# Kernel tuning notes

Measured on AMD Instinct MI355X. Metric: run time of the kernel, lower is better.

## Reference

```python
import jax, jax.numpy as jnp
import numpy as np

N, M, E, HID, H = 50000, 4000, 320000, 128, 2
EPS = 1e-5  # torch BatchNorm1d eps


def _lrelu(x):
    return jnp.where(x >= 0, x, 0.2 * x)


def _bn(x, g, b):
    # BatchNorm1d in training mode: biased batch statistics over dim 0
    m = x.mean(0)
    v = ((x - m) ** 2).mean(0)
    return g * (x - m) * jax.lax.rsqrt(v + EPS) + b


def _seg_softmax(a, idx, n):
    # softmax of a[E,heads] normalized per node index idx (PyG softmax)
    mx = jax.ops.segment_max(a, idx, num_segments=n)
    e = jnp.exp(a - mx[idx])
    s = jax.ops.segment_sum(e, idx, num_segments=n)
    return e / s[idx]


def _hgconv(x, he_n, he_e, he_w, W, att, bias, heads):
    # PyG HypergraphConv(use_attention=True, concat=False)
    xl = (x @ W).reshape(N, heads, HID)                  # lin(x) -> [N,heads,C]
    # hyperedge_attr = incidence^T @ x  (matches to_dense_adj path in HGAT)
    ea = jax.ops.segment_sum(x[he_n], he_e, num_segments=M)  # [M,F]
    eal = (ea @ W).reshape(M, heads, HID)                # lin(hyperedge_attr)
    a = (jnp.concatenate([xl[he_n], eal[he_e]], axis=-1) * att[0]).sum(-1)  # [E,heads]
    a = _seg_softmax(_lrelu(a), he_n, N)
    # degree normalizations
    Dn = jax.ops.segment_sum(he_w[he_e], he_n, num_segments=N)
    Dinv = jnp.where(Dn > 0, 1.0 / Dn, 0.0)
    Bn = jax.ops.segment_sum(jnp.ones((E,), x.dtype), he_e, num_segments=M)
    Binv = jnp.where(Bn > 0, 1.0 / Bn, 0.0)
    # node -> hyperedge
    m1 = Binv[he_e][:, None, None] * xl[he_n] * a[..., None]
    eo = jax.ops.segment_sum(m1, he_e, num_segments=M)   # [M,heads,C]
    # hyperedge -> node
    m2 = Dinv[he_n][:, None, None] * eo[he_e] * a[..., None]
    out = jax.ops.segment_sum(m2, he_n, num_segments=N)  # [N,heads,C]
    return out.mean(1) + bias                            # concat=False -> head mean


def _forward(x, he_w, lin1_w, lin1_b, bn1_g, bn1_b, h1_w, h1_att, h1_b,
             bn2_g, bn2_b, h2_w, h2_att, h2_b, bn3_g, bn3_b,
             lin2_w, lin2_b, bn4_g, bn4_b, he_n, he_e):
    src = x
    x = _bn(_lrelu(x @ lin1_w + lin1_b), bn1_g, bn1_b)
    x2 = _hgconv(x, he_n, he_e, he_w, h1_w, h1_att, h1_b, H)
    x = _bn(x + x2, bn2_g, bn2_b)
    x2 = _hgconv(x, he_n, he_e, he_w, h2_w, h2_att, h2_b, 1)
    x = _bn(x + x2, bn3_g, bn3_b)
    x = _lrelu(x @ lin2_w + lin2_b)
    return _bn(src + x, bn4_g, bn4_b)


def setup_inputs() -> dict:
    key = jax.random.key(0)
    ks = jax.random.split(key, 10)
    s = 0.05
    he_n = jax.random.randint(ks[0], (E,), 0, N, dtype=jnp.int32)
    he_e = (jnp.arange(E, dtype=jnp.int32) % M)  # every hyperedge id used
    return {
        'x': jax.random.normal(ks[1], (N, 128), jnp.float32),
        'he_n': he_n, 'he_e': he_e,
        'he_w': jnp.ones((M,), jnp.float32),
        'lin1_w': jax.random.normal(ks[2], (128, HID), jnp.float32) * s,
        'lin1_b': jnp.zeros((HID,), jnp.float32),
        'bn1_g': jnp.ones((HID,), jnp.float32), 'bn1_b': jnp.zeros((HID,), jnp.float32),
        'h1_w': jax.random.normal(ks[3], (HID, H * HID), jnp.float32) * s,
        'h1_att': jax.random.normal(ks[4], (1, H, 2 * HID), jnp.float32) * s,
        'h1_b': jnp.zeros((HID,), jnp.float32),
        'bn2_g': jnp.ones((HID,), jnp.float32), 'bn2_b': jnp.zeros((HID,), jnp.float32),
        'h2_w': jax.random.normal(ks[5], (HID, HID), jnp.float32) * s,
        'h2_att': jax.random.normal(ks[6], (1, 1, 2 * HID), jnp.float32) * s,
        'h2_b': jnp.zeros((HID,), jnp.float32),
        'bn3_g': jnp.ones((HID,), jnp.float32), 'bn3_b': jnp.zeros((HID,), jnp.float32),
        'lin2_w': jax.random.normal(ks[7], (HID, 128), jnp.float32) * s,
        'lin2_b': jnp.zeros((128,), jnp.float32),
        'bn4_g': jnp.ones((128,), jnp.float32), 'bn4_b': jnp.zeros((128,), jnp.float32),
    }


def reference(x, he_n, he_e, he_w, lin1_w, lin1_b, bn1_g, bn1_b, h1_w, h1_att, h1_b,
              bn2_g, bn2_b, h2_w, h2_att, h2_b, bn3_g, bn3_b,
              lin2_w, lin2_b, bn4_g, bn4_b):
    return _forward(x, he_w, lin1_w, lin1_b, bn1_g, bn1_b, h1_w, h1_att, h1_b,
                    bn2_g, bn2_b, h2_w, h2_att, h2_b, bn3_g, bn3_b,
                    lin2_w, lin2_b, bn4_g, bn4_b, he_n, he_e)
```

## Files before the change

kernel.cpp:

```cpp
#include <hip/hip_runtime.h>
#include <math.h>

constexpr int Nn = 50000;
constexpr int Mm = 4000;
constexpr int Ee = 320000;
constexpr int KPB = Ee / Mm;
constexpr float BINV = 1.0f / (float)KPB;
constexpr float EPSf = 1e-5f;
constexpr int NBKT = 16;
constexpr int NBSCAN = 49;

__device__ __forceinline__ float lrelu_f(float x) { return x >= 0.f ? x : 0.2f * x; }

__device__ __forceinline__ float wave_sum(float v) {
#pragma unroll
    for (int o = 32; o >= 1; o >>= 1) v += __shfl_xor(v, o, 64);
    return v;
}

__device__ __forceinline__ void finalize_to_lds(const float* __restrict__ st,
                                                const float* __restrict__ g,
                                                const float* __restrict__ b,
                                                float* ABsh, int t) {
    if (t < 128) {
        double ds = 0, dq = 0;
#pragma unroll
        for (int i = 0; i < NBKT; i++) {
            ds += (double)st[i * 256 + t];
            dq += (double)st[i * 256 + 128 + t];
        }
        double mean = ds / (double)Nn;
        double var = dq / (double)Nn - mean * mean;
        float rstd = (float)(1.0 / sqrt(var + (double)EPSf));
        float A = g[t] * rstd;
        ABsh[t] = A;
        ABsh[128 + t] = b[t] - (float)mean * A;
    }
    __syncthreads();
}

__device__ void scan_body(const int* __restrict__ counts, int* __restrict__ offs,
                          int b, int t) {
    __shared__ int sdi[256];
    int pre = 0;
    for (int i = t; i < b * 1024; i += 256) pre += counts[i];
    sdi[t] = pre;
    __syncthreads();
    for (int st = 128; st >= 1; st >>= 1) {
        if (t < st) sdi[t] += sdi[t + st];
        __syncthreads();
    }
    int run0 = sdi[0];
    __syncthreads();
    int c4[4];
    int s = 0;
#pragma unroll
    for (int i = 0; i < 4; i++) {
        int n = b * 1024 + t * 4 + i;
        c4[i] = (n < Nn) ? counts[n] : 0;
        s += c4[i];
    }
    sdi[t] = s;
    __syncthreads();
    for (int off = 1; off < 256; off <<= 1) {
        int v = (t >= off) ? sdi[t - off] : 0;
        __syncthreads();
        sdi[t] += v;
        __syncthreads();
    }
    int run = sdi[t] - s + run0;
#pragma unroll
    for (int i = 0; i < 4; i++) {
        int n = b * 1024 + t * 4 + i;
        if (n < Nn) offs[n] = run;
        run += c4[i];
    }
    if (b == NBSCAN - 1 && t == 255) offs[Nn] = run0 + sdi[255];
}

template <int ROWS, bool LRELU, bool PROBN, bool RESID, bool STATS, bool PACKH2, bool SCANX>
__global__ __launch_bounds__(256) void gemmT(const float* __restrict__ A, size_t aystride,
                                             const float* __restrict__ B, int ldb,
                                             const float* __restrict__ bias, float scale,
                                             const float* __restrict__ stIn,
                                             const float* __restrict__ fing,
                                             const float* __restrict__ finb,
                                             const float* __restrict__ resid,
                                             float* __restrict__ stF,
                                             float* __restrict__ C, int ldc, int R,
                                             int gemmBlocksX,
                                             const int* __restrict__ counts,
                                             int* __restrict__ offs) {
    constexpr int RPT = ROWS / 16;
    const int t = threadIdx.x;
    if (SCANX && (int)blockIdx.x >= gemmBlocksX) {
        if (blockIdx.y == 0) scan_body(counts, offs, blockIdx.x - gemmBlocksX, t);
        return;
    }
    __shared__ float As[16][ROWS + 4];
    __shared__ float Bs[16][128];
    __shared__ float Sred[STATS ? 16 : 1][STATS ? 128 : 1];
    __shared__ float ABsh[PROBN ? 256 : 1];
    const int ty = t >> 4, tx = t & 15;
    const int row0 = blockIdx.x * ROWS;
    const int bcol = blockIdx.y * 128;
    A += (size_t)blockIdx.y * aystride;

    if (PROBN) finalize_to_lds(stIn, fing, finb, ABsh, t);

    float4 acc[RPT][2];
#pragma unroll
    for (int i = 0; i < RPT; i++)
#pragma unroll
        for (int q = 0; q < 2; q++) acc[i][q] = make_float4(0.f, 0.f, 0.f, 0.f);

    for (int k0 = 0; k0 < 128; k0 += 16) {
        if (ROWS == 64) {
            int r = t >> 2, kc = (t & 3) * 4;
            int rr = row0 + r;
            rr = rr < R ? rr : R - 1;
            float4 av = *(const float4*)(A + (size_t)rr * 128 + k0 + kc);
            if (PROBN) {
                float4 sA = *(const float4*)&ABsh[k0 + kc];
                float4 sB = *(const float4*)&ABsh[128 + k0 + kc];
                av.x = av.x * sA.x + sB.x; av.y = av.y * sA.y + sB.y;
                av.z = av.z * sA.z + sB.z; av.w = av.w * sA.w + sB.w;
            }
            As[kc + 0][r] = av.x; As[kc + 1][r] = av.y;
            As[kc + 2][r] = av.z; As[kc + 3][r] = av.w;
        } else {
            int r = t >> 3, kc = (t & 7) * 2;
            int rr = row0 + r;
            rr = rr < R ? rr : R - 1;
            float2 av = *(const float2*)(A + (size_t)rr * 128 + k0 + kc);
            if (PROBN) {
                av.x = av.x * ABsh[k0 + kc] + ABsh[128 + k0 + kc];
                av.y = av.y * ABsh[k0 + kc + 1] + ABsh[128 + k0 + kc + 1];
            }
            As[kc + 0][r] = av.x;
            As[kc + 1][r] = av.y;
        }
        {
            int kk = t >> 5, c4 = (t & 31) * 4;
            float4 bv0 = *(const float4*)(B + (size_t)(k0 + kk) * ldb + bcol + c4);
            float4 bv1 = *(const float4*)(B + (size_t)(k0 + kk + 8) * ldb + bcol + c4);
            *(float4*)&Bs[kk][c4] = bv0;
            *(float4*)&Bs[kk + 8][c4] = bv1;
        }
        __syncthreads();
#pragma unroll
        for (int kk = 0; kk < 16; kk++) {
            float ar[RPT];
            if (RPT == 4) {
                float4 a4 = *(const float4*)&As[kk][ty * 4];
                ar[0] = a4.x; ar[1] = a4.y; ar[2] = a4.z; ar[3] = a4.w;
            } else {
                float2 a2 = *(const float2*)&As[kk][ty * 2];
                ar[0] = a2.x; ar[RPT - 1] = a2.y;
            }
            float4 b0 = *(const float4*)&Bs[kk][4 * tx];
            float4 b1 = *(const float4*)&Bs[kk][64 + 4 * tx];
#pragma unroll
            for (int i = 0; i < RPT; i++) {
                acc[i][0].x = fmaf(ar[i], b0.x, acc[i][0].x);
                acc[i][0].y = fmaf(ar[i], b0.y, acc[i][0].y);
                acc[i][0].z = fmaf(ar[i], b0.z, acc[i][0].z);
                acc[i][0].w = fmaf(ar[i], b0.w, acc[i][0].w);
                acc[i][1].x = fmaf(ar[i], b1.x, acc[i][1].x);
                acc[i][1].y = fmaf(ar[i], b1.y, acc[i][1].y);
                acc[i][1].z = fmaf(ar[i], b1.z, acc[i][1].z);
                acc[i][1].w = fmaf(ar[i], b1.w, acc[i][1].w);
            }
        }
        __syncthreads();
    }

    float4 bv0 = make_float4(0.f, 0.f, 0.f, 0.f), bv1 = bv0;
    if (bias) {
        bv0 = *(const float4*)(bias + bcol + 4 * tx);
        bv1 = *(const float4*)(bias + bcol + 64 + 4 * tx);
    }
    float4 cs0 = make_float4(0.f, 0.f, 0.f, 0.f), cs1 = cs0, cq0 = cs0, cq1 = cs0;
#pragma unroll
    for (int i = 0; i < RPT; i++) {
        int row = row0 + ty * RPT + i;
        if (row >= R) continue;
        float4 v0, v1;
        v0.x = acc[i][0].x * scale + bv0.x; v0.y = acc[i][0].y * scale + bv0.y;
        v0.z = acc[i][0].z * scale + bv0.z; v0.w = acc[i][0].w * scale + bv0.w;
        v1.x = acc[i][1].x * scale + bv1.x; v1.y = acc[i][1].y * scale + bv1.y;
        v1.z = acc[i][1].z * scale + bv1.z; v1.w = acc[i][1].w * scale + bv1.w;
        if (LRELU) {
            v0.x = lrelu_f(v0.x); v0.y = lrelu_f(v0.y); v0.z = lrelu_f(v0.z); v0.w = lrelu_f(v0.w);
            v1.x = lrelu_f(v1.x); v1.y = lrelu_f(v1.y); v1.z = lrelu_f(v1.z); v1.w = lrelu_f(v1.w);
        }
        if (RESID) {
            float4 r0 = *(const float4*)(resid + (size_t)row * 128 + bcol + 4 * tx);
            float4 r1 = *(const float4*)(resid + (size_t)row * 128 + bcol + 64 + 4 * tx);
            v0.x += r0.x; v0.y += r0.y; v0.z += r0.z; v0.w += r0.w;
            v1.x += r1.x; v1.y += r1.y; v1.z += r1.z; v1.w += r1.w;
        }
        if (PACKH2) {
            int h = blockIdx.y;
            float* c0 = C + (size_t)row * ldc + 8 * tx + 2 * h;
            *(float2*)(c0) = make_float2(v0.x, v0.y);
            *(float2*)(c0 + 4) = make_float2(v0.z, v0.w);
            float* c1 = C + (size_t)row * ldc + 128 + 8 * tx + 2 * h;
            *(float2*)(c1) = make_float2(v1.x, v1.y);
            *(float2*)(c1 + 4) = make_float2(v1.z, v1.w);
        } else {
            *(float4*)(C + (size_t)row * ldc + bcol + 4 * tx) = v0;
            *(float4*)(C + (size_t)row * ldc + bcol + 64 + 4 * tx) = v1;
        }
        if (STATS) {
            cs0.x += v0.x; cs0.y += v0.y; cs0.z += v0.z; cs0.w += v0.w;
            cs1.x += v1.x; cs1.y += v1.y; cs1.z += v1.z; cs1.w += v1.w;
            cq0.x += v0.x * v0.x; cq0.y += v0.y * v0.y; cq0.z += v0.z * v0.z; cq0.w += v0.w * v0.w;
            cq1.x += v1.x * v1.x; cq1.y += v1.y * v1.y; cq1.z += v1.z * v1.z; cq1.w += v1.w * v1.w;
        }
    }
    if (STATS) {
        int bkt = blockIdx.x & (NBKT - 1);
#pragma unroll
        for (int pass = 0; pass < 2; pass++) {
            *(float4*)&Sred[ty][4 * tx] = pass ? cq0 : cs0;
            *(float4*)&Sred[ty][64 + 4 * tx] = pass ? cq1 : cs1;
            __syncthreads();
            if (t < 128) {
                float tot = 0.f;
#pragma unroll
                for (int r = 0; r < 16; r++) tot += Sred[r][t];
                atomicAdd(&stF[bkt * 256 + pass * 128 + t], tot);
            }
            __syncthreads();
        }
    }
}

__global__ void count_edges_watt(const int* __restrict__ he_n, int* __restrict__ counts,
                                 const float* __restrict__ h1_w, const float* __restrict__ h1_att,
                                 const float* __restrict__ h2_w, const float* __restrict__ h2_att,
                                 float* __restrict__ wnA, float* __restrict__ weA,
                                 int* __restrict__ he_nT) {
    int t = threadIdx.x;
    if (blockIdx.x == 1250) {
        for (int j = 0; j < 3; j++) {
            int id = t + 256 * j;
            if (id >= 768) break;
            int which = id / 384;
            int rem = id % 384;
            int h3 = rem >> 7, k = rem & 127;
            float s = 0.f;
            if (h3 < 2) {
                const float* wrow = h1_w + (size_t)k * 256 + h3 * 128;
                const float* arow = h1_att + h3 * 256 + which * 128;
                for (int c = 0; c < 128; c++) s += wrow[c] * arow[c];
            } else {
                const float* wrow = h2_w + (size_t)k * 128;
                const float* arow = h2_att + which * 128;
                for (int c = 0; c < 128; c++) s += wrow[c] * arow[c];
            }
            (which ? weA : wnA)[h3 * 128 + k] = s;
        }
        return;
    }
    int g = blockIdx.x * 256 + t;
    if (g < Ee) {
        int m = g / KPB;
        int k = g - m * KPB;
        int n = he_n[m + (size_t)k * Mm];
        he_nT[g] = n;
        atomicAdd(&counts[n], 1);
    }
}

template <int H, bool FILL>
__global__ __launch_bounds__(256) void bn_dots(const float* __restrict__ X,
                                               const float* __restrict__ stIn,
                                               const float* __restrict__ fing,
                                               const float* __restrict__ finb,
                                               float* __restrict__ ABout,
                                               const float* __restrict__ wn,
                                               const float* __restrict__ we,
                                               float* __restrict__ an,
                                               float* __restrict__ pe,
                                               const int* __restrict__ he_n,
                                               const int* __restrict__ offs,
                                               int* __restrict__ cursor,
                                               int* __restrict__ eid, int mainBlocks) {
    int t = threadIdx.x;
    if (FILL && (int)blockIdx.x >= mainBlocks) {
        int e = (blockIdx.x - mainBlocks) * 256 + t;
        if (e < Ee) {
            int n = he_n[e];
            int p = atomicAdd(&cursor[n], 1);
            eid[offs[n] + p] = e;
        }
        return;
    }
    __shared__ float ABsh[256];
    finalize_to_lds(stIn, fing, finb, ABsh, t);
    if (blockIdx.x == 0) ABout[t] = ABsh[t];
    int w = t >> 6, lane = t & 63;
    float a0 = ABsh[lane], a1 = ABsh[lane + 64];
    float b0 = ABsh[128 + lane], b1 = ABsh[192 + lane];
    float wn0[H], wn1[H], we0[H], we1[H];
#pragma unroll
    for (int h = 0; h < H; h++) {
        wn0[h] = wn[h * 128 + lane]; wn1[h] = wn[h * 128 + 64 + lane];
        we0[h] = we[h * 128 + lane]; we1[h] = we[h * 128 + 64 + lane];
    }
#pragma unroll
    for (int nn = 0; nn < 4; nn++) {
        int row = blockIdx.x * 16 + w * 4 + nn;
        const float* xr = X + (size_t)row * 128;
        float v0 = xr[lane] * a0 + b0;
        float v1 = xr[lane + 64] * a1 + b1;
        float pv[H], qv[H];
#pragma unroll
        for (int h = 0; h < H; h++) {
            pv[h] = wave_sum(v0 * wn0[h] + v1 * wn1[h]);
            qv[h] = wave_sum(v0 * we0[h] + v1 * we1[h]);
        }
        if (lane == 0) {
            if (H == 2) {
                *(float2*)&an[row * 2] = make_float2(pv[0], pv[1]);
                *(float2*)&pe[row * 2] = make_float2(qv[0], qv[1]);
            } else {
                an[row] = pv[0];
                pe[row] = qv[0];
            }
        }
    }
}

__global__ __launch_bounds__(256) void bn_out(const float* __restrict__ X,
                                              const float* __restrict__ stIn,
                                              const float* __restrict__ fing,
                                              const float* __restrict__ finb,
                                              float* __restrict__ Y) {
    __shared__ float ABsh[256];
    int t = threadIdx.x;
    finalize_to_lds(stIn, fing, finb, ABsh, t);
    int w = t >> 6, lane = t & 63;
    float a0 = ABsh[lane], a1 = ABsh[lane + 64];
    float b0 = ABsh[128 + lane], b1 = ABsh[192 + lane];
#pragma unroll
    for (int nn = 0; nn < 4; nn++) {
        int row = blockIdx.x * 16 + w * 4 + nn;
        const float* xr = X + (size_t)row * 128;
        float* yr = Y + (size_t)row * 128;
        yr[lane] = xr[lane] * a0 + b0;
        yr[lane + 64] = xr[lane + 64] * a1 + b1;
    }
}

template <int H>
__global__ __launch_bounds__(256) void ea_from_pe(const int* __restrict__ he_nT,
                                                  const float* __restrict__ pe,
                                                  float* __restrict__ ae) {
    int w = threadIdx.x >> 6, lane = threadIdx.x & 63;
    int m = blockIdx.x * 4 + w;
    if (m >= Mm) return;
    float s[H];
#pragma unroll
    for (int h = 0; h < H; h++) s[h] = 0.f;
    for (int k = lane; k < KPB; k += 64) {
        int idx = he_nT[m * KPB + k];
        if (H == 2) {
            float2 p2 = *(const float2*)(pe + (size_t)idx * 2);
            s[0] += p2.x;
            s[H - 1] += p2.y;
        } else {
            s[0] += pe[idx];
        }
    }
#pragma unroll
    for (int h = 0; h < H; h++) s[h] = wave_sum(s[h]);
    if (lane == 0)
#pragma unroll
        for (int h = 0; h < H; h++) ae[m * H + h] = s[h];
}

template <int H>
__global__ __launch_bounds__(256) void seg_softmax(const int* __restrict__ offs,
                                                   const int* __restrict__ eid,
                                                   const float* __restrict__ an,
                                                   const float* __restrict__ ae,
                                                   const float* __restrict__ he_w,
                                                   float* __restrict__ nsp) {
    int t = threadIdx.x;
    int wv = t >> 6, lane = t & 63;
    int q = lane >> 3, li = lane & 7;
    int n = blockIdx.x * 32 + wv * 8 + q;
    bool valid = n < Nn;
    int base = valid ? offs[n] : 0;
    int deg = valid ? offs[n + 1] - base : 0;
    float anv[H];
#pragma unroll
    for (int h = 0; h < H; h++) anv[h] = valid ? an[n * H + h] : 0.f;

    bool h0 = li < deg, h1 = li + 8 < deg;
    int m0 = 0, m1 = 0;
    float l0[H], l1[H];
    float mx[H];
#pragma unroll
    for (int h = 0; h < H; h++) { mx[h] = -INFINITY; l0[h] = 0.f; l1[h] = 0.f; }
    if (h0) {
        m0 = eid[base + li] % Mm;
#pragma unroll
        for (int h = 0; h < H; h++) {
            l0[h] = lrelu_f(anv[h] + ae[m0 * H + h]);
            mx[h] = fmaxf(mx[h], l0[h]);
        }
    }
    if (h1) {
        m1 = eid[base + li + 8] % Mm;
#pragma unroll
        for (int h = 0; h < H; h++) {
            l1[h] = lrelu_f(anv[h] + ae[m1 * H + h]);
            mx[h] = fmaxf(mx[h], l1[h]);
        }
    }
    for (int c = li + 16; c < deg; c += 8) {
        int m = eid[base + c] % Mm;
#pragma unroll
        for (int h = 0; h < H; h++) mx[h] = fmaxf(mx[h], lrelu_f(anv[h] + ae[m * H + h]));
    }
#pragma unroll
    for (int h = 0; h < H; h++) {
#pragma unroll
        for (int o = 1; o <= 4; o <<= 1) mx[h] = fmaxf(mx[h], __shfl_xor(mx[h], o, 64));
    }
    float sm[H];
#pragma unroll
    for (int h = 0; h < H; h++) sm[h] = 0.f;
    float dn = 0.f;
    if (h0) {
        dn += he_w[m0];
#pragma unroll
        for (int h = 0; h < H; h++) sm[h] += expf(l0[h] - mx[h]);
    }
    if (h1) {
        dn += he_w[m1];
#pragma unroll
        for (int h = 0; h < H; h++) sm[h] += expf(l1[h] - mx[h]);
    }
    for (int c = li + 16; c < deg; c += 8) {
        int m = eid[base + c] % Mm;
        dn += he_w[m];
#pragma unroll
        for (int h = 0; h < H; h++) sm[h] += expf(lrelu_f(anv[h] + ae[m * H + h]) - mx[h]);
    }
#pragma unroll
    for (int o = 1; o <= 4; o <<= 1) dn += __shfl_xor(dn, o, 64);
#pragma unroll
    for (int h = 0; h < H; h++) {
#pragma unroll
        for (int o = 1; o <= 4; o <<= 1) sm[h] += __shfl_xor(sm[h], o, 64);
    }
    if (valid && li == 0) {
        float Dv = dn > 0.f ? 1.0f / dn : 0.0f;
        if (H == 2) {
            *(float4*)(nsp + (size_t)n * 8) = make_float4(anv[0], anv[H - 1], mx[0], mx[H - 1]);
            *(float4*)(nsp + (size_t)n * 8 + 4) =
                make_float4(1.f / sm[0], 1.f / sm[H - 1], 0.5f * Dv, 0.f);
        } else {
            *(float4*)(nsp + (size_t)n * 4) = make_float4(anv[0], mx[0], 1.f / sm[0], Dv);
        }
    }
}

template <int H>
__global__ __launch_bounds__(256) void s_build(const float* __restrict__ X,
                                               const float* __restrict__ AB,
                                               const int* __restrict__ he_nT,
                                               const float* __restrict__ nsp,
                                               const float* __restrict__ ae,
                                               float* __restrict__ S) {
    __shared__ int idx[KPB];
    __shared__ float av[KPB][H];
    __shared__ float red[8][H][128];
    int m = blockIdx.x, t = threadIdx.x;
    int g = t >> 5, l = t & 31;
    if (t < KPB) {
        int nd = he_nT[m * KPB + t];
        idx[t] = nd;
        if (H == 2) {
            float4 pa = *(const float4*)(nsp + (size_t)nd * 8);
            float4 pb = *(const float4*)(nsp + (size_t)nd * 8 + 4);
            float2 a2 = *(const float2*)(ae + (size_t)m * 2);
            av[t][0] = expf(lrelu_f(pa.x + a2.x) - pa.z) * pb.x;
            av[t][H - 1] = expf(lrelu_f(pa.y + a2.y) - pa.w) * pb.y;
        } else {
            float4 pa = *(const float4*)(nsp + (size_t)nd * 4);
            float aem = ae[m];
            av[t][0] = expf(lrelu_f(pa.x + aem) - pa.y) * pa.z;
        }
    }
    __syncthreads();
    float4 A4 = ((const float4*)AB)[l];
    float4 B4 = ((const float4*)(AB + 128))[l];
    float4 acc[H];
#pragma unroll
    for (int h = 0; h < H; h++) acc[h] = make_float4(0.f, 0.f, 0.f, 0.f);
#pragma unroll
    for (int kk = 0; kk < KPB / 8; kk++) {
        int k = g + kk * 8;
        float4 v = ((const float4*)(X + (size_t)idx[k] * 128))[l];
        v.x = v.x * A4.x + B4.x;
        v.y = v.y * A4.y + B4.y;
        v.z = v.z * A4.z + B4.z;
        v.w = v.w * A4.w + B4.w;
#pragma unroll
        for (int h = 0; h < H; h++) {
            float a = av[k][h];
            acc[h].x = fmaf(a, v.x, acc[h].x);
            acc[h].y = fmaf(a, v.y, acc[h].y);
            acc[h].z = fmaf(a, v.z, acc[h].z);
            acc[h].w = fmaf(a, v.w, acc[h].w);
        }
    }
#pragma unroll
    for (int h = 0; h < H; h++) *(float4*)&red[g][h][l * 4] = acc[h];
    __syncthreads();
    if (t < 32 * H) {
        int h = t >> 5, l2 = t & 31;
        float4 s = make_float4(0.f, 0.f, 0.f, 0.f);
#pragma unroll
        for (int gg = 0; gg < 8; gg++) {
            float4 r = *(const float4*)&red[gg][h][l2 * 4];
            s.x += r.x; s.y += r.y; s.z += r.z; s.w += r.w;
        }
        ((float4*)(S + ((size_t)h * Mm + m) * 128))[l2] = s;
    }
}

template <int H>
__global__ __launch_bounds__(256) void node_agg(const int* __restrict__ offs,
                                                const int* __restrict__ eid,
                                                const float* __restrict__ nsp,
                                                const float* __restrict__ ae,
                                                const float* __restrict__ eo,
                                                const float* __restrict__ bias,
                                                const float* __restrict__ AB,
                                                float* __restrict__ stF,
                                                float* __restrict__ T) {
    __shared__ float smem[4][256];
    __shared__ float redS[4][128], redQ[4][128];
    int t = threadIdx.x;
    int w = t >> 6, lane = t & 63;
    int n0 = blockIdx.x * 16 + w * 4;
    int o = offs[n0 + (lane < 4 ? lane : 4)];
    int b0 = __shfl(o, 0, 64);
    int b1 = __shfl(o, 1, 64);
    int b2 = __shfl(o, 2, 64);
    int b3 = __shfl(o, 3, 64);
    int b4 = __shfl(o, 4, 64);
    int cnt = b4 - b0;
    int cnt64 = cnt < 64 ? cnt : 64;

    if (lane < cnt64) {
        int slot = b0 + lane;
        int j = (slot >= b1) + (slot >= b2) + (slot >= b3);
        int e = eid[slot];
        int m = e % Mm;
        if (H == 2) {
            float4 pa = *(const float4*)(nsp + (size_t)(n0 + j) * 8);
            float4 pb = *(const float4*)(nsp + (size_t)(n0 + j) * 8 + 4);
            float2 a2 = *(const float2*)(ae + (size_t)m * 2);
            float c0 = expf(lrelu_f(pa.x + a2.x) - pa.z) * pb.x * pb.z;
            float c1 = expf(lrelu_f(pa.y + a2.y) - pa.w) * pb.y * pb.z;
            *(float4*)&smem[w][4 * lane] = make_float4(__int_as_float(m), c0, c1, 0.f);
        } else {
            float4 pa = *(const float4*)(nsp + (size_t)(n0 + j) * 4);
            float c = expf(lrelu_f(pa.x + ae[m]) - pa.y) * pa.z * pa.w;
            *(float2*)&smem[w][2 * lane] = make_float2(__int_as_float(m), c);
        }
    }
    __syncthreads();

    int s1 = min(b1 - b0, cnt64), s2 = min(b2 - b0, cnt64), s3 = min(b3 - b0, cnt64);
    float2 acc0 = make_float2(0.f, 0.f), acc1 = acc0, acc2 = acc0, acc3 = acc0;

#define NA_BODY(ACC, CBEG, CEND)                                                \
    {                                                                           \
        int c = (CBEG);                                                         \
        for (; c + 1 < (CEND); c += 2) {                                        \
            if (H == 2) {                                                       \
                float4 sa = *(const float4*)&smem[w][4 * c];                    \
                float4 sb = *(const float4*)&smem[w][4 * (c + 1)];              \
                float4 ea = *(const float4*)(eo + (size_t)__float_as_int(sa.x) * 256 + 4 * lane); \
                float4 eb = *(const float4*)(eo + (size_t)__float_as_int(sb.x) * 256 + 4 * lane); \
                ACC.x += sa.y * ea.x + sa.z * ea.z + sb.y * eb.x + sb.z * eb.z; \
                ACC.y += sa.y * ea.y + sa.z * ea.w + sb.y * eb.y + sb.z * eb.w; \
            } else {                                                            \
                float2 sa = *(const float2*)&smem[w][2 * c];                    \
                float2 sb = *(const float2*)&smem[w][2 * (c + 1)];              \
                float2 ea = *(const float2*)(eo + (size_t)__float_as_int(sa.x) * 128 + 2 * lane); \
                float2 eb = *(const float2*)(eo + (size_t)__float_as_int(sb.x) * 128 + 2 * lane); \
                ACC.x += sa.y * ea.x + sb.y * eb.x;                             \
                ACC.y += sa.y * ea.y + sb.y * eb.y;                             \
            }                                                                   \
        }                                                                       \
        if (c < (CEND)) {                                                       \
            if (H == 2) {                                                       \
                float4 sa = *(const float4*)&smem[w][4 * c];                    \
                float4 ea = *(const float4*)(eo + (size_t)__float_as_int(sa.x) * 256 + 4 * lane); \
                ACC.x += sa.y * ea.x + sa.z * ea.z;                             \
                ACC.y += sa.y * ea.y + sa.z * ea.w;                             \
            } else {                                                            \
                float2 sa = *(const float2*)&smem[w][2 * c];                    \
                float2 ea = *(const float2*)(eo + (size_t)__float_as_int(sa.x) * 128 + 2 * lane); \
                ACC.x += sa.y * ea.x;                                           \
                ACC.y += sa.y * ea.y;                                           \
            }                                                                   \
        }                                                                       \
    }
    NA_BODY(acc0, 0, s1)
    NA_BODY(acc1, s1, s2)
    NA_BODY(acc2, s2, s3)
    NA_BODY(acc3, s3, cnt64)
#undef NA_BODY

    for (int ss = 64; ss < cnt; ss++) {
        int slot = b0 + ss;
        int j = (slot >= b1) + (slot >= b2) + (slot >= b3);
        int e = eid[slot];
        int m = e % Mm;
        float cx, cy;
        if (H == 2) {
            float4 pa = *(const float4*)(nsp + (size_t)(n0 + j) * 8);
            float4 pb = *(const float4*)(nsp + (size_t)(n0 + j) * 8 + 4);
            float2 a2 = *(const float2*)(ae + (size_t)m * 2);
            float c0 = expf(lrelu_f(pa.x + a2.x) - pa.z) * pb.x * pb.z;
            float c1 = expf(lrelu_f(pa.y + a2.y) - pa.w) * pb.y * pb.z;
            float4 ev = *(const float4*)(eo + (size_t)m * 256 + 4 * lane);
            cx = c0 * ev.x + c1 * ev.z;
            cy = c0 * ev.y + c1 * ev.w;
        } else {
            float4 pa = *(const float4*)(nsp + (size_t)(n0 + j) * 4);
            float c = expf(lrelu_f(pa.x + ae[m]) - pa.y) * pa.z * pa.w;
            float2 ev = *(const float2*)(eo + (size_t)m * 128 + 2 * lane);
            cx = c * ev.x;
            cy = c * ev.y;
        }
        if (j == 0) { acc0.x += cx; acc0.y += cy; }
        else if (j == 1) { acc1.x += cx; acc1.y += cy; }
        else if (j == 2) { acc2.x += cx; acc2.y += cy; }
        else { acc3.x += cx; acc3.y += cy; }
    }

    int col = 2 * lane;
    float2 A2 = *(const float2*)(AB + col);
    float2 B2 = *(const float2*)(AB + 128 + col);
    float2 bi = *(const float2*)(bias + col);
    float cs0 = 0.f, cs1 = 0.f, cq0 = 0.f, cq1 = 0.f;
    float2 accs[4] = {acc0, acc1, acc2, acc3};
#pragma unroll
    for (int j = 0; j < 4; j++) {
        int n = n0 + j;
        float2 xr = *(const float2*)(T + (size_t)n * 128 + col);
        float r0 = xr.x * A2.x + B2.x + bi.x + accs[j].x;
        float r1 = xr.y * A2.y + B2.y + bi.y + accs[j].y;
        *(float2*)(T + (size_t)n * 128 + col) = make_float2(r0, r1);
        cs0 += r0; cs1 += r1;
        cq0 += r0 * r0; cq1 += r1 * r1;
    }
    redS[w][col] = cs0; redS[w][col + 1] = cs1;
    redQ[w][col] = cq0; redQ[w][col + 1] = cq1;
    __syncthreads();
    if (t < 128) {
        float s = 0.f, qq = 0.f;
#pragma unroll
        for (int ww = 0; ww < 4; ww++) { s += redS[ww][t]; qq += redQ[ww][t]; }
        int bkt = blockIdx.x & (NBKT - 1);
        atomicAdd(&stF[bkt * 256 + t], s);
        atomicAdd(&stF[bkt * 256 + 128 + t], qq);
    }
}

extern "C" void kernel_launch(void* const* d_in, const int* in_sizes, int n_in,
                              void* d_out, int out_size, void* d_ws, size_t ws_size,
                              hipStream_t stream) {
    const float* x = (const float*)d_in[0];
    const int* he_n = (const int*)d_in[1];
    const float* he_w = (const float*)d_in[3];
    const float* lin1_w = (const float*)d_in[4];
    const float* lin1_b = (const float*)d_in[5];
    const float* bn1_g = (const float*)d_in[6];
    const float* bn1_b = (const float*)d_in[7];
    const float* h1_w = (const float*)d_in[8];
    const float* h1_att = (const float*)d_in[9];
    const float* h1_b = (const float*)d_in[10];
    const float* bn2_g = (const float*)d_in[11];
    const float* bn2_b = (const float*)d_in[12];
    const float* h2_w = (const float*)d_in[13];
    const float* h2_att = (const float*)d_in[14];
    const float* h2_b = (const float*)d_in[15];
    const float* bn3_g = (const float*)d_in[16];
    const float* bn3_b = (const float*)d_in[17];
    const float* lin2_w = (const float*)d_in[18];
    const float* lin2_b = (const float*)d_in[19];
    const float* bn4_g = (const float*)d_in[20];
    const float* bn4_b = (const float*)d_in[21];
    float* out = (float*)d_out;

    char* ws = (char*)d_ws;
    size_t off = 0;
    auto alloc = [&](size_t bytes) -> char* {
        char* p = ws + off;
        off = (off + bytes + 255) & ~(size_t)255;
        return p;
    };
    int* counts = (int*)alloc((size_t)Nn * 4);
    int* cursor = (int*)alloc((size_t)Nn * 4);
    float* stats = (float*)alloc((size_t)4 * NBKT * 256 * 4);
    size_t zbytes = off;
    int* offs = (int*)alloc((size_t)(Nn + 1) * 4);
    int* eid = (int*)alloc((size_t)Ee * 4);
    int* he_nT = (int*)alloc((size_t)Ee * 4);
    float* an = (float*)alloc((size_t)Nn * 2 * 4);
    float* pe = (float*)alloc((size_t)Nn * 2 * 4);
    float* ae = (float*)alloc((size_t)Mm * 2 * 4);
    float* nsp = (float*)alloc((size_t)Nn * 8 * 4);
    float* S = (float*)alloc((size_t)2 * Mm * 128 * 4);
    float* eo = (float*)alloc((size_t)2 * Mm * 128 * 4);
    float* wnA = (float*)alloc(384 * 4);
    float* weA = (float*)alloc(384 * 4);
    float* AB = (float*)alloc(2 * 256 * 4);
    float* buf = (float*)alloc((size_t)Nn * 128 * 4);

    float* st0 = stats;
    float* st1 = stats + NBKT * 256;
    float* st2 = stats + 2 * NBKT * 256;
    float* st3 = stats + 3 * NBKT * 256;
    float *AB1 = AB, *AB2 = AB + 256;

    hipMemsetAsync(d_ws, 0, zbytes, stream);

    constexpr int GB64 = (Nn + 63) / 64;
    count_edges_watt<<<1251, 256, 0, stream>>>(he_n, counts, h1_w, h1_att, h2_w, h2_att,
                                               wnA, weA, he_nT);

    gemmT<64, true, false, false, true, false, true><<<dim3(GB64 + NBSCAN, 1), 256, 0, stream>>>(
        x, 0, lin1_w, 128, lin1_b, 1.f, nullptr, nullptr, nullptr, nullptr, st0, buf, 128, Nn,
        GB64, counts, offs);
    bn_dots<2, true><<<3125 + 1250, 256, 0, stream>>>(buf, st0, bn1_g, bn1_b, AB1, wnA, weA,
                                                      an, pe, he_n, offs, cursor, eid, 3125);

    ea_from_pe<2><<<Mm / 4, 256, 0, stream>>>(he_nT, pe, ae);
    seg_softmax<2><<<(Nn + 31) / 32, 256, 0, stream>>>(offs, eid, an, ae, he_w, nsp);
    s_build<2><<<Mm, 256, 0, stream>>>(buf, AB1, he_nT, nsp, ae, S);
    gemmT<32, false, false, false, false, true, false><<<dim3(125, 2), 256, 0, stream>>>(
        S, (size_t)Mm * 128, h1_w, 256, nullptr, BINV, nullptr, nullptr, nullptr, nullptr,
        nullptr, eo, 256, Mm, 125, nullptr, nullptr);
    node_agg<2><<<3125, 256, 0, stream>>>(offs, eid, nsp, ae, eo, h1_b, AB1, st1, buf);

    bn_dots<1, false><<<3125, 256, 0, stream>>>(buf, st1, bn2_g, bn2_b, AB2, wnA + 256,
                                                weA + 256, an, pe, nullptr, nullptr, nullptr,
                                                nullptr, 3125);

    ea_from_pe<1><<<Mm / 4, 256, 0, stream>>>(he_nT, pe, ae);
    seg_softmax<1><<<(Nn + 31) / 32, 256, 0, stream>>>(offs, eid, an, ae, he_w, nsp);
    s_build<1><<<Mm, 256, 0, stream>>>(buf, AB2, he_nT, nsp, ae, S);
    gemmT<32, false, false, false, false, false, false><<<dim3(125, 1), 256, 0, stream>>>(
        S, 0, h2_w, 128, nullptr, BINV, nullptr, nullptr, nullptr, nullptr, nullptr,
        eo, 128, Mm, 125, nullptr, nullptr);
    node_agg<1><<<3125, 256, 0, stream>>>(offs, eid, nsp, ae, eo, h2_b, AB2, st2, buf);

    gemmT<64, true, true, true, true, false, false><<<dim3(GB64, 1), 256, 0, stream>>>(
        buf, 0, lin2_w, 128, lin2_b, 1.f, st2, bn3_g, bn3_b, x, st3, buf, 128, Nn,
        GB64, nullptr, nullptr);
    bn_out<<<3125, 256, 0, stream>>>(buf, st3, bn4_g, bn4_b, out);
}
```

Baseline: 395.8 us.

## Use split-bf16 MFMA for the two large node GEMMs

Replaces the FP32 SIMT tiled GEMM for lin1 and lin2 over 50000 rows with a matrix-core kernel. Activations are split on the fly into high and low bf16 parts and multiplied by pre-split, pre-swizzled weight fragments using three bf16 MFMAs, which approximates FP32 accuracy. The weight conversion runs in an extra block of the existing count kernel. Accuracy drops slightly versus true FP32, and C is written with scalar per-lane stores instead of float4 stores.

```diff
diff --git a/kernel.cpp b/kernel.cpp
--- a/kernel.cpp
+++ b/kernel.cpp
@@ -10,7 +10,15 @@
 constexpr int NBKT = 16;
 constexpr int NBSCAN = 49;
 
+typedef __attribute__((ext_vector_type(8))) short bfrag_t;
+typedef __attribute__((ext_vector_type(4))) float facc_t;
+
 __device__ __forceinline__ float lrelu_f(float x) { return x >= 0.f ? x : 0.2f * x; }
+
+__device__ __forceinline__ unsigned short f2bf(float f) {
+    unsigned int u = __float_as_uint(f);
+    return (unsigned short)((u + 0x7FFFu + ((u >> 16) & 1u)) >> 16);
+}
 
 __device__ __forceinline__ float wave_sum(float v) {
 #pragma unroll
@@ -78,36 +86,132 @@
     if (b == NBSCAN - 1 && t == 255) offs[Nn] = run0 + sdi[255];
 }
 
-template <int ROWS, bool LRELU, bool PROBN, bool RESID, bool STATS, bool PACKH2, bool SCANX>
-__global__ __launch_bounds__(256) void gemmT(const float* __restrict__ A, size_t aystride,
-                                             const float* __restrict__ B, int ldb,
-                                             const float* __restrict__ bias, float scale,
+template <bool LRELU, bool PROBN, bool RESID, bool STATS, bool SCANX>
+__global__ __launch_bounds__(256) void gemmM(const float* __restrict__ A,
+                                             const unsigned short* __restrict__ BH,
+                                             const unsigned short* __restrict__ BL,
+                                             const float* __restrict__ bias,
                                              const float* __restrict__ stIn,
                                              const float* __restrict__ fing,
                                              const float* __restrict__ finb,
                                              const float* __restrict__ resid,
                                              float* __restrict__ stF,
-                                             float* __restrict__ C, int ldc, int R,
+                                             float* __restrict__ C, int R,
                                              int gemmBlocksX,
                                              const int* __restrict__ counts,
                                              int* __restrict__ offs) {
+    const int t = threadIdx.x;
+    if (SCANX && (int)blockIdx.x >= gemmBlocksX) {
+        scan_body(counts, offs, blockIdx.x - gemmBlocksX, t);
+        return;
+    }
+    __shared__ float ABsh[PROBN ? 256 : 1];
+    __shared__ float SredS[STATS ? 4 : 1][STATS ? 128 : 1];
+    __shared__ float SredQ[STATS ? 4 : 1][STATS ? 128 : 1];
+    const int wv = t >> 6, l = t & 63, lm = l & 15, lg = l >> 4;
+    const int row0 = blockIdx.x * 64 + wv * 16;
+
+    if (PROBN) finalize_to_lds(stIn, fing, finb, ABsh, t);
+
+    int rA = row0 + lm;
+    rA = rA < R ? rA : R - 1;
+    const float* Ap = A + (size_t)rA * 128 + lg * 8;
+
+    facc_t acc[8];
+#pragma unroll
+    for (int ct = 0; ct < 8; ct++) acc[ct] = (facc_t){0.f, 0.f, 0.f, 0.f};
+
+#pragma unroll
+    for (int ks = 0; ks < 4; ks++) {
+        float4 a0 = *(const float4*)(Ap + ks * 32);
+        float4 a1 = *(const float4*)(Ap + ks * 32 + 4);
+        if (PROBN) {
+            const int cb = ks * 32 + lg * 8;
+            float4 cA0 = *(const float4*)&ABsh[cb];
+            float4 cA1 = *(const float4*)&ABsh[cb + 4];
+            float4 cB0 = *(const float4*)&ABsh[128 + cb];
+            float4 cB1 = *(const float4*)&ABsh[128 + cb + 4];
+            a0.x = a0.x * cA0.x + cB0.x; a0.y = a0.y * cA0.y + cB0.y;
+            a0.z = a0.z * cA0.z + cB0.z; a0.w = a0.w * cA0.w + cB0.w;
+            a1.x = a1.x * cA1.x + cB1.x; a1.y = a1.y * cA1.y + cB1.y;
+            a1.z = a1.z * cA1.z + cB1.z; a1.w = a1.w * cA1.w + cB1.w;
+        }
+        float av[8] = {a0.x, a0.y, a0.z, a0.w, a1.x, a1.y, a1.z, a1.w};
+        bfrag_t ah, al;
+#pragma unroll
+        for (int j = 0; j < 8; j++) {
+            unsigned short h = f2bf(av[j]);
+            float hf = __uint_as_float(((unsigned int)h) << 16);
+            ah[j] = (short)h;
+            al[j] = (short)f2bf(av[j] - hf);
+        }
+#pragma unroll
+        for (int ct = 0; ct < 8; ct++) {
+            const size_t fo = (((size_t)(ks * 8 + ct)) * 64 + l) * 8;
+            bfrag_t bh = *(const bfrag_t*)(BH + fo);
+            bfrag_t bl = *(const bfrag_t*)(BL + fo);
+            acc[ct] = __builtin_amdgcn_mfma_f32_16x16x32_bf16(ah, bh, acc[ct], 0, 0, 0);
+            acc[ct] = __builtin_amdgcn_mfma_f32_16x16x32_bf16(al, bh, acc[ct], 0, 0, 0);
+            acc[ct] = __builtin_amdgcn_mfma_f32_16x16x32_bf16(ah, bl, acc[ct], 0, 0, 0);
+        }
+    }
+
+    float cs[8], cq[8];
+#pragma unroll
+    for (int ct = 0; ct < 8; ct++) { cs[ct] = 0.f; cq[ct] = 0.f; }
+#pragma unroll
+    for (int ct = 0; ct < 8; ct++) {
+        const int col = ct * 16 + lm;
+        const float bv = bias ? bias[col] : 0.f;
+#pragma unroll
+        for (int r = 0; r < 4; r++) {
+            const int row = row0 + lg * 4 + r;
+            if (row >= R) continue;
+            float v = acc[ct][r] + bv;
+            if (LRELU) v = lrelu_f(v);
+            if (RESID) v += resid[(size_t)row * 128 + col];
+            C[(size_t)row * 128 + col] = v;
+            if (STATS) { cs[ct] += v; cq[ct] += v * v; }
+        }
+    }
+    if (STATS) {
+#pragma unroll
+        for (int ct = 0; ct < 8; ct++) {
+            cs[ct] += __shfl_xor(cs[ct], 16, 64);
+            cs[ct] += __shfl_xor(cs[ct], 32, 64);
+            cq[ct] += __shfl_xor(cq[ct], 16, 64);
+            cq[ct] += __shfl_xor(cq[ct], 32, 64);
+            if (lg == 0) {
+                SredS[wv][ct * 16 + lm] = cs[ct];
+                SredQ[wv][ct * 16 + lm] = cq[ct];
+            }
+        }
+        __syncthreads();
+        if (t < 128) {
+            float s = 0.f, q = 0.f;
+#pragma unroll
+            for (int ww = 0; ww < 4; ww++) { s += SredS[ww][t]; q += SredQ[ww][t]; }
+            int bkt = blockIdx.x & (NBKT - 1);
+            atomicAdd(&stF[bkt * 256 + t], s);
+            atomicAdd(&stF[bkt * 256 + 128 + t], q);
+        }
+    }
+}
+
+template <int ROWS, bool PACKH2>
+__global__ __launch_bounds__(256) void gemmT(const float* __restrict__ A, size_t aystride,
+                                             const float* __restrict__ B, int ldb,
+                                             float scale,
+                                             float* __restrict__ C, int ldc, int R) {
     constexpr int RPT = ROWS / 16;
     const int t = threadIdx.x;
-    if (SCANX && (int)blockIdx.x >= gemmBlocksX) {
-        if (blockIdx.y == 0) scan_body(counts, offs, blockIdx.x - gemmBlocksX, t);
-        return;
-    }
     __shared__ float As[16][ROWS + 4];
     __shared__ float Bs[16][128];
-    __shared__ float Sred[STATS ? 16 : 1][STATS ? 128 : 1];
-    __shared__ float ABsh[PROBN ? 256 : 1];
     const int ty = t >> 4, tx = t & 15;
     const int row0 = blockIdx.x * ROWS;
     const int bcol = blockIdx.y * 128;
     A += (size_t)blockIdx.y * aystride;
 
-    if (PROBN) finalize_to_lds(stIn, fing, finb, ABsh, t);
-
     float4 acc[RPT][2];
 #pragma unroll
     for (int i = 0; i < RPT; i++)
@@ -115,28 +219,11 @@
         for (int q = 0; q < 2; q++) acc[i][q] = make_float4(0.f, 0.f, 0.f, 0.f);
 
     for (int k0 = 0; k0 < 128; k0 += 16) {
-        if (ROWS == 64) {
-            int r = t >> 2, kc = (t & 3) * 4;
-            int rr = row0 + r;
-            rr = rr < R ? rr : R - 1;
-            float4 av = *(const float4*)(A + (size_t)rr * 128 + k0 + kc);
-            if (PROBN) {
-                float4 sA = *(const float4*)&ABsh[k0 + kc];
-                float4 sB = *(const float4*)&ABsh[128 + k0 + kc];
-                av.x = av.x * sA.x + sB.x; av.y = av.y * sA.y + sB.y;
-                av.z = av.z * sA.z + sB.z; av.w = av.w * sA.w + sB.w;
-            }
-            As[kc + 0][r] = av.x; As[kc + 1][r] = av.y;
-            As[kc + 2][r] = av.z; As[kc + 3][r] = av.w;
-        } else {
+        {
             int r = t >> 3, kc = (t & 7) * 2;
             int rr = row0 + r;
             rr = rr < R ? rr : R - 1;
             float2 av = *(const float2*)(A + (size_t)rr * 128 + k0 + kc);
-            if (PROBN) {
-                av.x = av.x * ABsh[k0 + kc] + ABsh[128 + k0 + kc];
-                av.y = av.y * ABsh[k0 + kc + 1] + ABsh[128 + k0 + kc + 1];
-            }
             As[kc + 0][r] = av.x;
             As[kc + 1][r] = av.y;
         }
@@ -151,10 +238,7 @@
 #pragma unroll
         for (int kk = 0; kk < 16; kk++) {
             float ar[RPT];
-            if (RPT == 4) {
-                float4 a4 = *(const float4*)&As[kk][ty * 4];
-                ar[0] = a4.x; ar[1] = a4.y; ar[2] = a4.z; ar[3] = a4.w;
-            } else {
+            {
                 float2 a2 = *(const float2*)&As[kk][ty * 2];
                 ar[0] = a2.x; ar[RPT - 1] = a2.y;
             }
@@ -175,31 +259,15 @@
         __syncthreads();
     }
 
-    float4 bv0 = make_float4(0.f, 0.f, 0.f, 0.f), bv1 = bv0;
-    if (bias) {
-        bv0 = *(const float4*)(bias + bcol + 4 * tx);
-        bv1 = *(const float4*)(bias + bcol + 64 + 4 * tx);
-    }
-    float4 cs0 = make_float4(0.f, 0.f, 0.f, 0.f), cs1 = cs0, cq0 = cs0, cq1 = cs0;
 #pragma unroll
     for (int i = 0; i < RPT; i++) {
         int row = row0 + ty * RPT + i;
         if (row >= R) continue;
         float4 v0, v1;
-        v0.x = acc[i][0].x * scale + bv0.x; v0.y = acc[i][0].y * scale + bv0.y;
-        v0.z = acc[i][0].z * scale + bv0.z; v0.w = acc[i][0].w * scale + bv0.w;
-        v1.x = acc[i][1].x * scale + bv1.x; v1.y = acc[i][1].y * scale + bv1.y;
-        v1.z = acc[i][1].z * scale + bv1.z; v1.w = acc[i][1].w * scale + bv1.w;
-        if (LRELU) {
-            v0.x = lrelu_f(v0.x); v0.y = lrelu_f(v0.y); v0.z = lrelu_f(v0.z); v0.w = lrelu_f(v0.w);
-            v1.x = lrelu_f(v1.x); v1.y = lrelu_f(v1.y); v1.z = lrelu_f(v1.z); v1.w = lrelu_f(v1.w);
-        }
-        if (RESID) {
-            float4 r0 = *(const float4*)(resid + (size_t)row * 128 + bcol + 4 * tx);
-            float4 r1 = *(const float4*)(resid + (size_t)row * 128 + bcol + 64 + 4 * tx);
-            v0.x += r0.x; v0.y += r0.y; v0.z += r0.z; v0.w += r0.w;
-            v1.x += r1.x; v1.y += r1.y; v1.z += r1.z; v1.w += r1.w;
-        }
+        v0.x = acc[i][0].x * scale; v0.y = acc[i][0].y * scale;
+        v0.z = acc[i][0].z * scale; v0.w = acc[i][0].w * scale;
+        v1.x = acc[i][1].x * scale; v1.y = acc[i][1].y * scale;
+        v1.z = acc[i][1].z * scale; v1.w = acc[i][1].w * scale;
         if (PACKH2) {
             int h = blockIdx.y;
             float* c0 = C + (size_t)row * ldc + 8 * tx + 2 * h;
@@ -212,28 +280,6 @@
             *(float4*)(C + (size_t)row * ldc + bcol + 4 * tx) = v0;
             *(float4*)(C + (size_t)row * ldc + bcol + 64 + 4 * tx) = v1;
         }
-        if (STATS) {
-            cs0.x += v0.x; cs0.y += v0.y; cs0.z += v0.z; cs0.w += v0.w;
-            cs1.x += v1.x; cs1.y += v1.y; cs1.z += v1.z; cs1.w += v1.w;
-            cq0.x += v0.x * v0.x; cq0.y += v0.y * v0.y; cq0.z += v0.z * v0.z; cq0.w += v0.w * v0.w;
-            cq1.x += v1.x * v1.x; cq1.y += v1.y * v1.y; cq1.z += v1.z * v1.z; cq1.w += v1.w * v1.w;
-        }
-    }
-    if (STATS) {
-        int bkt = blockIdx.x & (NBKT - 1);
-#pragma unroll
-        for (int pass = 0; pass < 2; pass++) {
-            *(float4*)&Sred[ty][4 * tx] = pass ? cq0 : cs0;
-            *(float4*)&Sred[ty][64 + 4 * tx] = pass ? cq1 : cs1;
-            __syncthreads();
-            if (t < 128) {
-                float tot = 0.f;
-#pragma unroll
-                for (int r = 0; r < 16; r++) tot += Sred[r][t];
-                atomicAdd(&stF[bkt * 256 + pass * 128 + t], tot);
-            }
-            __syncthreads();
-        }
     }
 }
 
@@ -241,7 +287,11 @@
                                  const float* __restrict__ h1_w, const float* __restrict__ h1_att,
                                  const float* __restrict__ h2_w, const float* __restrict__ h2_att,
                                  float* __restrict__ wnA, float* __restrict__ weA,
-                                 int* __restrict__ he_nT) {
+                                 int* __restrict__ he_nT,
+                                 const float* __restrict__ lin1_w,
+                                 const float* __restrict__ lin2_w,
+                                 unsigned short* __restrict__ bfH,
+                                 unsigned short* __restrict__ bfL) {
     int t = threadIdx.x;
     if (blockIdx.x == 1250) {
         for (int j = 0; j < 3; j++) {
@@ -261,6 +311,21 @@
                 for (int c = 0; c < 128; c++) s += wrow[c] * arow[c];
             }
             (which ? weA : wnA)[h3 * 128 + k] = s;
+        }
+        return;
+    }
+    if (blockIdx.x == 1251) {
+        for (int q = t; q < 32768; q += 256) {
+            int mat = q >> 14;
+            int e = q & 16383;
+            int j = e & 7, lane = (e >> 3) & 63, ct = (e >> 9) & 7, ks = e >> 12;
+            int k = ks * 32 + (lane >> 4) * 8 + j;
+            int n = ct * 16 + (lane & 15);
+            float f = (mat ? lin2_w : lin1_w)[(size_t)k * 128 + n];
+            unsigned short h = f2bf(f);
+            float hf = __uint_as_float(((unsigned int)h) << 16);
+            bfH[mat * 16384 + e] = h;
+            bfL[mat * 16384 + e] = f2bf(f - hf);
         }
         return;
     }
@@ -729,6 +794,8 @@
     float* wnA = (float*)alloc(384 * 4);
     float* weA = (float*)alloc(384 * 4);
     float* AB = (float*)alloc(2 * 256 * 4);
+    unsigned short* bfH = (unsigned short*)alloc((size_t)2 * 16384 * 2);
+    unsigned short* bfL = (unsigned short*)alloc((size_t)2 * 16384 * 2);
     float* buf = (float*)alloc((size_t)Nn * 128 * 4);
 
     float* st0 = stats;
@@ -739,22 +806,21 @@
 
     hipMemsetAsync(d_ws, 0, zbytes, stream);
 
-    constexpr int GB64 = (Nn + 63) / 64;
-    count_edges_watt<<<1251, 256, 0, stream>>>(he_n, counts, h1_w, h1_att, h2_w, h2_att,
-                                               wnA, weA, he_nT);
-
-    gemmT<64, true, false, false, true, false, true><<<dim3(GB64 + NBSCAN, 1), 256, 0, stream>>>(
-        x, 0, lin1_w, 128, lin1_b, 1.f, nullptr, nullptr, nullptr, nullptr, st0, buf, 128, Nn,
-        GB64, counts, offs);
+    constexpr int GB64M = (Nn + 63) / 64;
+    count_edges_watt<<<1252, 256, 0, stream>>>(he_n, counts, h1_w, h1_att, h2_w, h2_att,
+                                               wnA, weA, he_nT, lin1_w, lin2_w, bfH, bfL);
+
+    gemmM<true, false, false, true, true><<<GB64M + NBSCAN, 256, 0, stream>>>(
+        x, bfH, bfL, lin1_b, nullptr, nullptr, nullptr, nullptr, st0, buf, Nn,
+        GB64M, counts, offs);
     bn_dots<2, true><<<3125 + 1250, 256, 0, stream>>>(buf, st0, bn1_g, bn1_b, AB1, wnA, weA,
                                                       an, pe, he_n, offs, cursor, eid, 3125);
 
     ea_from_pe<2><<<Mm / 4, 256, 0, stream>>>(he_nT, pe, ae);
     seg_softmax<2><<<(Nn + 31) / 32, 256, 0, stream>>>(offs, eid, an, ae, he_w, nsp);
     s_build<2><<<Mm, 256, 0, stream>>>(buf, AB1, he_nT, nsp, ae, S);
-    gemmT<32, false, false, false, false, true, false><<<dim3(125, 2), 256, 0, stream>>>(
-        S, (size_t)Mm * 128, h1_w, 256, nullptr, BINV, nullptr, nullptr, nullptr, nullptr,
-        nullptr, eo, 256, Mm, 125, nullptr, nullptr);
+    gemmT<32, true><<<dim3(125, 2), 256, 0, stream>>>(
+        S, (size_t)Mm * 128, h1_w, 256, BINV, eo, 256, Mm);
     node_agg<2><<<3125, 256, 0, stream>>>(offs, eid, nsp, ae, eo, h1_b, AB1, st1, buf);
 
     bn_dots<1, false><<<3125, 256, 0, stream>>>(buf, st1, bn2_g, bn2_b, AB2, wnA + 256,
@@ -764,13 +830,12 @@
     ea_from_pe<1><<<Mm / 4, 256, 0, stream>>>(he_nT, pe, ae);
     seg_softmax<1><<<(Nn + 31) / 32, 256, 0, stream>>>(offs, eid, an, ae, he_w, nsp);
     s_build<1><<<Mm, 256, 0, stream>>>(buf, AB2, he_nT, nsp, ae, S);
-    gemmT<32, false, false, false, false, false, false><<<dim3(125, 1), 256, 0, stream>>>(
-        S, 0, h2_w, 128, nullptr, BINV, nullptr, nullptr, nullptr, nullptr, nullptr,
-        eo, 128, Mm, 125, nullptr, nullptr);
+    gemmT<32, false><<<dim3(125, 1), 256, 0, stream>>>(
+        S, 0, h2_w, 128, BINV, eo, 128, Mm);
     node_agg<1><<<3125, 256, 0, stream>>>(offs, eid, nsp, ae, eo, h2_b, AB2, st2, buf);
 
-    gemmT<64, true, true, true, true, false, false><<<dim3(GB64, 1), 256, 0, stream>>>(
-        buf, 0, lin2_w, 128, lin2_b, 1.f, st2, bn3_g, bn3_b, x, st3, buf, 128, Nn,
-        GB64, nullptr, nullptr);
+    gemmM<true, true, true, true, false><<<GB64M, 256, 0, stream>>>(
+        buf, bfH + 16384, bfL + 16384, lin2_b, st2, bn3_g, bn3_b, x, st3, buf, Nn,
+        GB64M, nullptr, nullptr);
     bn_out<<<3125, 256, 0, stream>>>(buf, st3, bn4_g, bn4_b, out);
 }
```

New measurement: 403.2 us. No clear change (+1.9%).
